# Performance work log

Hardware: AMD Instinct MI355X
Metric: run time of the kernel (lower is better)

Reference implementation:

```python
import jax, jax.numpy as jnp
import numpy as np

PARENTS = np.array([-1, 0, 1, 1, 1])
NECK_CHAIN = np.array([1, 0])  # neck joint (1) up to root (0)
B, V, F, J, S, E = 512, 5023, 9976, 5, 100, 50
L_STAT, L_DYN, L_FULL, N_BUCKET = 51, 17, 68, 79


def rodrigues(rvec):
    """Axis-angle [N,3] -> rotation matrices [N,3,3]."""
    angle = jnp.linalg.norm(rvec + 1e-8, axis=-1, keepdims=True)  # [N,1]
    axis = rvec / angle
    s = jnp.sin(angle)[..., None]
    c = jnp.cos(angle)[..., None]
    rx, ry, rz = axis[:, 0], axis[:, 1], axis[:, 2]
    z = jnp.zeros_like(rx)
    K = jnp.stack([z, -rz, ry, rz, z, -rx, -ry, rx, z], axis=-1).reshape(-1, 3, 3)
    I = jnp.eye(3, dtype=rvec.dtype)
    return I + s * K + (1.0 - c) * (K @ K)


def verts2lmk(vertices, faces, lmk_faces_idx, lmk_bary):
    lmk_faces = faces[lmk_faces_idx]                               # [B,L,3]
    lmk_verts = jax.vmap(lambda v, f: v[f])(vertices, lmk_faces)   # [B,L,3verts,3xyz]
    return jnp.einsum('blfc,blf->blc', lmk_verts, lmk_bary)


def setup_inputs() -> dict:
    key = jax.random.key(0)
    ks = jax.random.split(key, 16)
    shape_params = jax.random.normal(ks[0], (B, S), jnp.float32)
    expression_params = jax.random.normal(ks[1], (B, E), jnp.float32)
    pose_params = 0.2 * jax.random.normal(ks[2], (B, 6), jnp.float32)
    eye_pose_params = 0.1 * jax.random.normal(ks[3], (B, 6), jnp.float32)
    v_template = jax.random.normal(ks[4], (V, 3), jnp.float32) * 0.1
    shapedirs = jax.random.normal(ks[5], (V, 3, S + E), jnp.float32) * 0.01
    posedirs = jax.random.normal(ks[6], ((J - 1) * 9, V * 3), jnp.float32) * 0.01
    jr = jax.random.uniform(ks[7], (J, V), jnp.float32)
    J_regressor = jr / jnp.sum(jr, axis=1, keepdims=True)
    lbs_weights = jax.nn.softmax(jax.random.normal(ks[8], (V, J), jnp.float32), axis=-1)
    faces = jax.random.randint(ks[9], (F, 3), 0, V)
    lmk_faces_idx = jax.random.randint(ks[10], (L_STAT,), 0, F)
    lb = jax.random.uniform(ks[11], (L_STAT, 3), jnp.float32) + 1e-3
    lmk_bary_coords = lb / jnp.sum(lb, axis=-1, keepdims=True)
    dynamic_lmk_faces_idx = jax.random.randint(ks[12], (N_BUCKET, L_DYN), 0, F)
    db = jax.random.uniform(ks[13], (N_BUCKET, L_DYN, 3), jnp.float32) + 1e-3
    dynamic_lmk_bary_coords = db / jnp.sum(db, axis=-1, keepdims=True)
    full_lmk_faces_idx = jax.random.randint(ks[14], (L_FULL,), 0, F)
    fb = jax.random.uniform(ks[15], (L_FULL, 3), jnp.float32) + 1e-3
    full_lmk_bary_coords = fb / jnp.sum(fb, axis=-1, keepdims=True)
    return {
        'shape_params': shape_params, 'expression_params': expression_params,
        'pose_params': pose_params, 'eye_pose_params': eye_pose_params,
        'v_template': v_template, 'shapedirs': shapedirs, 'posedirs': posedirs,
        'J_regressor': J_regressor, 'lbs_weights': lbs_weights, 'faces': faces,
        'lmk_faces_idx': lmk_faces_idx, 'lmk_bary_coords': lmk_bary_coords,
        'dynamic_lmk_faces_idx': dynamic_lmk_faces_idx,
        'dynamic_lmk_bary_coords': dynamic_lmk_bary_coords,
        'full_lmk_faces_idx': full_lmk_faces_idx,
        'full_lmk_bary_coords': full_lmk_bary_coords,
    }


def reference(shape_params, expression_params, pose_params, eye_pose_params,
              v_template, shapedirs, posedirs, J_regressor, lbs_weights, faces,
              lmk_faces_idx, lmk_bary_coords, dynamic_lmk_faces_idx,
              dynamic_lmk_bary_coords, full_lmk_faces_idx, full_lmk_bary_coords):
    b = shape_params.shape[0]
    nv = v_template.shape[0]
    dt = shape_params.dtype
    betas = jnp.concatenate([shape_params, expression_params], axis=1)          # [B,150]
    neck = jnp.zeros((b, 3), dtype=dt)
    full_pose = jnp.concatenate(
        [pose_params[:, :3], neck, pose_params[:, 3:], eye_pose_params], axis=1)  # [B,15]
    # shape + expression blendshapes
    v_shaped = v_template[None] + jnp.einsum('bl,vcl->bvc', betas, shapedirs)   # [B,V,3]
    joints = jnp.einsum('jv,bvc->bjc', J_regressor, v_shaped)                   # [B,5,3]
    rot_mats = rodrigues(full_pose.reshape(-1, 3)).reshape(b, J, 3, 3)          # [B,5,3,3]
    I3 = jnp.eye(3, dtype=dt)
    pose_feature = (rot_mats[:, 1:] - I3).reshape(b, -1)                        # [B,36]
    v_posed = v_shaped + (pose_feature @ posedirs).reshape(b, nv, 3)
    # kinematic chain -> global joint transforms
    rel_J = joints.at[:, 1:].add(-joints[:, PARENTS[1:]])
    tm = jnp.zeros((b, J, 4, 4), dtype=dt)
    tm = tm.at[:, :, :3, :3].set(rot_mats).at[:, :, :3, 3].set(rel_J).at[:, :, 3, 3].set(1.0)
    chain = [tm[:, 0]]
    for i in range(1, J):
        chain.append(chain[PARENTS[i]] @ tm[:, i])
    A = jnp.stack(chain, axis=1)                                                # [B,5,4,4]
    Rj = jnp.einsum('bjmn,bjn->bjm', A[:, :, :3, :3], joints)
    A_rel = A.at[:, :, :3, 3].add(-Rj)
    # per-vertex skinning
    T = jnp.einsum('vj,bjmn->bvmn', lbs_weights, A_rel)                         # [B,V,4,4]
    vertices = jnp.einsum('bvmn,bvn->bvm', T[:, :, :3, :3], v_posed) + T[:, :, :3, 3]
    # dynamic contour landmark selection from neck kin-chain relative rotation
    aa = full_pose.reshape(b, J, 3)[:, NECK_CHAIN]                              # [B,2,3]
    rc = rodrigues(aa.reshape(-1, 3)).reshape(b, len(NECK_CHAIN), 3, 3)
    rel_rot = jnp.broadcast_to(I3, (b, 3, 3))
    for idx in range(len(NECK_CHAIN)):
        rel_rot = rc[:, idx] @ rel_rot
    sy = jnp.sqrt(rel_rot[:, 0, 0] ** 2 + rel_rot[:, 1, 0] ** 2)
    y_deg = jnp.arctan2(-rel_rot[:, 2, 0], sy) * (180.0 / np.pi)
    y_rot = jnp.round(jnp.minimum(y_deg, 39.0)).astype(jnp.int32)
    neg_mask = y_rot < 0
    big_neg = y_rot < -39
    neg_vals = jnp.where(big_neg, 78, 39 - y_rot)
    y_rot = jnp.where(neg_mask, neg_vals, y_rot)                                # [B] in [0,79)
    dyn_faces = dynamic_lmk_faces_idx[y_rot]                                    # [B,17]
    dyn_bary = dynamic_lmk_bary_coords[y_rot]                                   # [B,17,3]
    lf = jnp.concatenate([dyn_faces, jnp.broadcast_to(lmk_faces_idx[None], (b, lmk_faces_idx.shape[0]))], axis=1)
    lb = jnp.concatenate([dyn_bary, jnp.broadcast_to(lmk_bary_coords[None], (b,) + lmk_bary_coords.shape)], axis=1)
    landmarks2d = verts2lmk(vertices, faces, lf, lb)
    ff = jnp.broadcast_to(full_lmk_faces_idx[None], (b, full_lmk_faces_idx.shape[0]))
    fb = jnp.broadcast_to(full_lmk_bary_coords[None], (b,) + full_lmk_bary_coords.shape)
    landmarks3d = verts2lmk(vertices, faces, ff, fb)
    return (vertices, landmarks2d, landmarks3d)
```

## Files before the change

### kernel.cpp

```cpp
#include <hip/hip_runtime.h>
#include <cstddef>
#include <cstdint>

#define cB   512
#define cV   5023
#define cS   100
#define cE   50
#define cJ   5
#define cLD  17
#define cLF  68

#define cV3    15069
#define cNPAD  15072

#define OUT_V  ((size_t)cB * cV * 3)
#define OUT_L  ((size_t)cB * cLF * 3)

#define WS_BTN    ((size_t)0)
#define WS_ATM    (WS_BTN + (size_t)cNPAD * 96)
#define WS_JS2    (WS_ATM + 49152)
#define WS_AREL   (WS_JS2 + 2432)
#define WS_YROT   (WS_AREL + 30720)
#define WS_JSPART (WS_YROT + 512)

typedef __attribute__((ext_vector_type(8))) short short8;
typedef __attribute__((ext_vector_type(4))) float f32x4;

__device__ __forceinline__ unsigned short f2bf(float x) {
  unsigned int u = __float_as_uint(x);
  u = (u + 0x7fffu + ((u >> 16) & 1u)) >> 16;
  return (unsigned short)u;
}

__device__ __forceinline__ void rodrigues9(float rx, float ry, float rz, float* R) {
  float a0 = rx + 1e-8f, a1 = ry + 1e-8f, a2 = rz + 1e-8f;
  float angle = sqrtf(a0 * a0 + a1 * a1 + a2 * a2);
  float inv = 1.0f / angle;
  float x = rx * inv, y = ry * inv, z = rz * inv;
  float s = sinf(angle), c = cosf(angle);
  float t = 1.0f - c;
  float xy = x * y, xz = x * z, yz = y * z;
  R[0] = 1.0f - t * (y * y + z * z);
  R[1] = -s * z + t * xy;
  R[2] =  s * y + t * xz;
  R[3] =  s * z + t * xy;
  R[4] = 1.0f - t * (x * x + z * z);
  R[5] = -s * x + t * yz;
  R[6] = -s * y + t * xz;
  R[7] =  s * x + t * yz;
  R[8] = 1.0f - t * (x * x + y * y);
}

__global__ __launch_bounds__(512) void k_aux(
    const float* __restrict__ sd, const float* __restrict__ pd,
    const float* __restrict__ jreg, const float* __restrict__ vt,
    unsigned int* __restrict__ btn_u, float* __restrict__ JSpart) {
  __shared__ __align__(16) unsigned char sm[44032];
  float* sdt = (float*)sm;
  unsigned short* pdt = (unsigned short*)(sm + 38912);
  const int t = threadIdx.x;
  const int bid = blockIdx.x;
  if (bid < 314) {
    if (t >= 453) return;
    int c = t / 151, l = t - c * 151;
    int v0 = bid * 16;
    float acc[5] = {0.f, 0.f, 0.f, 0.f, 0.f};
#pragma unroll 8
    for (int vi = 0; vi < 16; ++vi) {
      int v = v0 + vi;
      bool ok = (v < cV);
      int vc = ok ? v : 0;
      float x;
      if (l < 150) x = ok ? sd[(size_t)(v * 3 + c) * 150 + l] : 0.f;
      else         x = ok ? vt[v * 3 + c] : 0.f;
#pragma unroll
      for (int j = 0; j < 5; ++j)
        acc[j] = fmaf(jreg[j * cV + vc], x, acc[j]);
    }
#pragma unroll
    for (int j = 0; j < 5; ++j)
      JSpart[(size_t)bid * 2272 + (j * 3 + c) * 151 + l] = acc[j];
  } else {
    const int n0 = (bid - 314) * 64;
    for (int idx = t; idx < 9600; idx += 512) {
      size_t g = (size_t)n0 * 150 + idx;
      float v = (g < (size_t)cV3 * 150) ? sd[g] : 0.f;
      int row = idx / 150, col = idx - row * 150;
      sdt[row * 152 + col] = v;
    }
    for (int e = t; e < 2304; e += 512) {
      int kk = e >> 6, ln = e & 63;
      int n = n0 + ln;
      pdt[ln * 38 + kk] = f2bf((n < cV3) ? pd[(size_t)kk * cV3 + n] : 0.f);
    }
    __syncthreads();
    for (int e = t; e < 6144; e += 512) {
      int row = e / 96, d = e - row * 96;
      int n = n0 + row;
      if (n < cNPAD) {
        unsigned int wv;
        if (d < 75) {
          wv = (unsigned int)f2bf(sdt[row * 152 + 2 * d]) |
               ((unsigned int)f2bf(sdt[row * 152 + 2 * d + 1]) << 16);
        } else if (d < 93) {
          int p = (d - 75) * 2;
          wv = (unsigned int)pdt[row * 38 + p] |
               ((unsigned int)pdt[row * 38 + p + 1] << 16);
        } else {
          wv = 0u;
        }
        btn_u[(size_t)n * 96 + d] = wv;
      }
    }
  }
}

__global__ __launch_bounds__(256) void k_jsred(const float* __restrict__ JSpart,
                                               float* __restrict__ JS2) {
  __shared__ float red[256];
  const int t = threadIdx.x;
  const int e = blockIdx.x * 32 + (t & 31);
  const int pg = t >> 5;
  float s = 0.f;
  if (e < 2265) {
#pragma unroll 8
    for (int p = pg; p < 314; p += 8)
      s += JSpart[(size_t)p * 2272 + e];
  }
  red[t] = s;
  __syncthreads();
  if (t < 128) red[t] += red[t + 128];
  __syncthreads();
  if (t < 64) red[t] += red[t + 64];
  __syncthreads();
  if (t < 32) {
    float v = red[t] + red[t + 32];
    if (e < 2265) {
      int jc = e / 151, l = e - jc * 151;
      JS2[l * 16 + jc] = v;
    }
  }
}

__global__ __launch_bounds__(256) void k_batch(
    const float* __restrict__ shp, const float* __restrict__ expr,
    const float* __restrict__ pose, const float* __restrict__ eyep,
    const float* __restrict__ JS2g, float* __restrict__ Arel,
    int* __restrict__ yrot, unsigned int* __restrict__ atm_u) {
  __shared__ float js2[151 * 16];
  __shared__ float sb[32 * 153];
  __shared__ float pfs[32 * 36];
  const int t = threadIdx.x;
  const int b0 = blockIdx.x * 32;
  for (int i = t; i < 151 * 16; i += 256) js2[i] = JS2g[i];
  for (int e = t; e < 3200; e += 256) {
    int bl = e / 100, l = e - bl * 100;
    sb[bl * 153 + l] = shp[(size_t)(b0 + bl) * 100 + l];
  }
  for (int e = t; e < 1600; e += 256) {
    int bl = e / 50, l = e - bl * 50;
    sb[bl * 153 + 100 + l] = expr[(size_t)(b0 + bl) * 50 + l];
  }
  __syncthreads();

  if (t < 32) {
    int b = b0 + t;
    float jnt[5][3];
    {
      const f32x4* J4 = (const f32x4*)(js2 + 150 * 16);
      f32x4 A = J4[0], Bq = J4[1], Cq = J4[2], Dq = J4[3];
      jnt[0][0] = A.x;  jnt[0][1] = A.y;  jnt[0][2] = A.z;
      jnt[1][0] = A.w;  jnt[1][1] = Bq.x; jnt[1][2] = Bq.y;
      jnt[2][0] = Bq.z; jnt[2][1] = Bq.w; jnt[2][2] = Cq.x;
      jnt[3][0] = Cq.y; jnt[3][1] = Cq.z; jnt[3][2] = Cq.w;
      jnt[4][0] = Dq.x; jnt[4][1] = Dq.y; jnt[4][2] = Dq.z;
    }
    for (int l = 0; l < 150; ++l) {
      const f32x4* J4 = (const f32x4*)(js2 + l * 16);
      f32x4 A = J4[0], Bq = J4[1], Cq = J4[2], Dq = J4[3];
      float beta = sb[t * 153 + l];
      jnt[0][0] = fmaf(beta, A.x,  jnt[0][0]);
      jnt[0][1] = fmaf(beta, A.y,  jnt[0][1]);
      jnt[0][2] = fmaf(beta, A.z,  jnt[0][2]);
      jnt[1][0] = fmaf(beta, A.w,  jnt[1][0]);
      jnt[1][1] = fmaf(beta, Bq.x, jnt[1][1]);
      jnt[1][2] = fmaf(beta, Bq.y, jnt[1][2]);
      jnt[2][0] = fmaf(beta, Bq.z, jnt[2][0]);
      jnt[2][1] = fmaf(beta, Bq.w, jnt[2][1]);
      jnt[2][2] = fmaf(beta, Cq.x, jnt[2][2]);
      jnt[3][0] = fmaf(beta, Cq.y, jnt[3][0]);
      jnt[3][1] = fmaf(beta, Cq.z, jnt[3][1]);
      jnt[3][2] = fmaf(beta, Cq.w, jnt[3][2]);
      jnt[4][0] = fmaf(beta, Dq.x, jnt[4][0]);
      jnt[4][1] = fmaf(beta, Dq.y, jnt[4][1]);
      jnt[4][2] = fmaf(beta, Dq.z, jnt[4][2]);
    }
    float fp[5][3];
    fp[0][0] = pose[b * 6 + 0]; fp[0][1] = pose[b * 6 + 1]; fp[0][2] = pose[b * 6 + 2];
    fp[1][0] = 0.f; fp[1][1] = 0.f; fp[1][2] = 0.f;
    fp[2][0] = pose[b * 6 + 3]; fp[2][1] = pose[b * 6 + 4]; fp[2][2] = pose[b * 6 + 5];
    fp[3][0] = eyep[b * 6 + 0]; fp[3][1] = eyep[b * 6 + 1]; fp[3][2] = eyep[b * 6 + 2];
    fp[4][0] = eyep[b * 6 + 3]; fp[4][1] = eyep[b * 6 + 4]; fp[4][2] = eyep[b * 6 + 5];
    float R[5][9];
#pragma unroll
    for (int j = 0; j < 5; ++j) rodrigues9(fp[j][0], fp[j][1], fp[j][2], R[j]);
#pragma unroll
    for (int j = 1; j < 5; ++j)
#pragma unroll
      for (int r = 0; r < 9; ++r) {
        float id = (r == 0 || r == 4 || r == 8) ? 1.f : 0.f;
        pfs[t * 36 + (j - 1) * 9 + r] = R[j][r] - id;
      }
    float rel[5][3];
#pragma unroll
    for (int c = 0; c < 3; ++c) {
      rel[0][c] = jnt[0][c];
      rel[1][c] = jnt[1][c] - jnt[0][c];
      rel[2][c] = jnt[2][c] - jnt[1][c];
      rel[3][c] = jnt[3][c] - jnt[1][c];
      rel[4][c] = jnt[4][c] - jnt[1][c];
    }
    float GR[5][9], Gt[5][3];
#pragma unroll
    for (int r = 0; r < 9; ++r) GR[0][r] = R[0][r];
#pragma unroll
    for (int c = 0; c < 3; ++c) Gt[0][c] = rel[0][c];
    const int par[5] = {0, 0, 1, 1, 1};
#pragma unroll
    for (int j = 1; j < 5; ++j) {
      int p = par[j];
#pragma unroll
      for (int r = 0; r < 3; ++r) {
#pragma unroll
        for (int cc = 0; cc < 3; ++cc)
          GR[j][r * 3 + cc] = GR[p][r * 3 + 0] * R[j][0 + cc] +
                              GR[p][r * 3 + 1] * R[j][3 + cc] +
                              GR[p][r * 3 + 2] * R[j][6 + cc];
        Gt[j][r] = Gt[p][r] + GR[p][r * 3 + 0] * rel[j][0] +
                              GR[p][r * 3 + 1] * rel[j][1] +
                              GR[p][r * 3 + 2] * rel[j][2];
      }
    }
#pragma unroll
    for (int j = 0; j < 5; ++j)
#pragma unroll
      for (int r = 0; r < 3; ++r) {
        float tj = Gt[j][r] - (GR[j][r * 3 + 0] * jnt[j][0] +
                               GR[j][r * 3 + 1] * jnt[j][1] +
                               GR[j][r * 3 + 2] * jnt[j][2]);
        Arel[b * 60 + j * 12 + r * 4 + 0] = GR[j][r * 3 + 0];
        Arel[b * 60 + j * 12 + r * 4 + 1] = GR[j][r * 3 + 1];
        Arel[b * 60 + j * 12 + r * 4 + 2] = GR[j][r * 3 + 2];
        Arel[b * 60 + j * 12 + r * 4 + 3] = tj;
      }
    float Ra[9], Rb[9];
    rodrigues9(fp[1][0], fp[1][1], fp[1][2], Ra);
    rodrigues9(fp[0][0], fp[0][1], fp[0][2], Rb);
    float r00 = Rb[0] * Ra[0] + Rb[1] * Ra[3] + Rb[2] * Ra[6];
    float r10 = Rb[3] * Ra[0] + Rb[4] * Ra[3] + Rb[5] * Ra[6];
    float r20 = Rb[6] * Ra[0] + Rb[7] * Ra[3] + Rb[8] * Ra[6];
    float sy = sqrtf(r00 * r00 + r10 * r10);
    float ydeg = atan2f(-r20, sy) * 57.29577951308232f;
    int y = (int)rintf(fminf(ydeg, 39.0f));
    if (y < 0) y = (y < -39) ? 78 : (39 - y);
    yrot[b] = y;
  }
  __syncthreads();

#pragma unroll
  for (int it = 0; it < 12; ++it) {
    int e = t + it * 256;
    int bl = e / 96, d = e - bl * 96;
    unsigned int wv;
    if (d < 75) {
      wv = (unsigned int)f2bf(sb[bl * 153 + 2 * d]) |
           ((unsigned int)f2bf(sb[bl * 153 + 2 * d + 1]) << 16);
    } else if (d < 93) {
      wv = (unsigned int)f2bf(pfs[bl * 36 + (d - 75) * 2]) |
           ((unsigned int)f2bf(pfs[bl * 36 + (d - 75) * 2 + 1]) << 16);
    } else {
      wv = 0u;
    }
    atm_u[(size_t)(b0 + bl) * 96 + d] = wv;
  }
}

__global__ __launch_bounds__(256) void k_main(
    const unsigned short* __restrict__ BTn, const unsigned short* __restrict__ ATm,
    const float* __restrict__ Arel, const float* __restrict__ vtempl,
    const float* __restrict__ lbw, float* __restrict__ out) {
  __shared__ __align__(16) unsigned char smem[39424];
  unsigned short* Bs = (unsigned short*)smem;
  float* Pf   = (float*)smem;
  float* lbwT = (float*)(smem + 38400);
  float* vtT  = (float*)(smem + 39040);

  const int bid = blockIdx.x;
  const int ph = bid >> 6, mb = (bid >> 3) & 7, r8 = bid & 7;
  const int p = ph * 8 + r8;

  const int t = threadIdx.x;
  const int w = t >> 6, L = t & 63;
  const int wm = w >> 1, wn = w & 1;
  const int lr = L & 15, lq = L >> 4;
  const int b_loc = t >> 2, part = t & 3;

  const float* qb = Arel + ((size_t)mb * 64 + b_loc) * 60;
  f32x4 ar[15];
#pragma unroll
  for (int r = 0; r < 15; ++r) ar[r] = *(const f32x4*)(qb + 4 * r);
  const unsigned short* abase = ATm + ((size_t)mb * 64 + wm * 32 + lr) * 192 + lq * 8;

#pragma unroll 1
  for (int i = 0; i < 2; ++i) {
    const int nb = 2 * p + i;
    if (nb >= 157) continue;
    if (i) __syncthreads();

    const unsigned short* bsrc = BTn + (size_t)nb * 96 * 192;
    uint4 bst[9];
#pragma unroll
    for (int it = 0; it < 9; ++it)
      bst[it] = *(const uint4*)(bsrc + ((size_t)(t + it * 256)) * 8);
#pragma unroll
    for (int it = 0; it < 9; ++it) {
      int e = t + it * 256;
      int row = e / 24, col = e - row * 24;
      *(uint4*)(smem + row * 400 + col * 16) = bst[it];
    }
    if (t < 160) {
      int vl = t / 5, j = t - vl * 5;
      int v = nb * 32 + vl;
      lbwT[t] = (v < cV) ? lbw[v * 5 + j] : 0.f;
    }
    if (t < 96) {
      int vl = t / 3, c = t - vl * 3;
      int v = nb * 32 + vl;
      vtT[t] = (v < cV) ? vtempl[v * 3 + c] : 0.f;
    }
    __syncthreads();

    f32x4 acc[2][3];
#pragma unroll
    for (int mt = 0; mt < 2; ++mt)
#pragma unroll
      for (int nt = 0; nt < 3; ++nt) acc[mt][nt] = (f32x4){0.f, 0.f, 0.f, 0.f};

    short8 af0 = *(const short8*)(abase);
    short8 af1 = *(const short8*)(abase + 16 * 192);
#pragma unroll
    for (int ks = 0; ks < 6; ++ks) {
      short8 nf0, nf1;
      if (ks < 5) {
        nf0 = *(const short8*)(abase + (ks + 1) * 32);
        nf1 = *(const short8*)(abase + 16 * 192 + (ks + 1) * 32);
      }
      const int ko = ks * 32 + lq * 8;
      short8 bf[3];
#pragma unroll
      for (int nt = 0; nt < 3; ++nt)
        bf[nt] = *(const short8*)(Bs + (wn * 48 + nt * 16 + lr) * 200 + ko);
#pragma unroll
      for (int nt = 0; nt < 3; ++nt) {
        acc[0][nt] = __builtin_amdgcn_mfma_f32_16x16x32_bf16(af0, bf[nt], acc[0][nt], 0, 0, 0);
        acc[1][nt] = __builtin_amdgcn_mfma_f32_16x16x32_bf16(af1, bf[nt], acc[1][nt], 0, 0, 0);
      }
      af0 = nf0; af1 = nf1;
    }
    __syncthreads();

#pragma unroll
    for (int mt = 0; mt < 2; ++mt)
#pragma unroll
      for (int nt = 0; nt < 3; ++nt) {
        int n_loc = wn * 48 + nt * 16 + lr;
        int m = wm * 32 + mt * 16 + lq * 4;
        *(f32x4*)(Pf + n_loc * 66 + m) = acc[mt][nt];
      }
    __syncthreads();

#pragma unroll
    for (int ii = 0; ii < 8; ++ii) {
      const int vl = part * 8 + ii;
      float px = Pf[(vl * 3 + 0) * 66 + b_loc] + vtT[vl * 3 + 0];
      float py = Pf[(vl * 3 + 1) * 66 + b_loc] + vtT[vl * 3 + 1];
      float pz = Pf[(vl * 3 + 2) * 66 + b_loc] + vtT[vl * 3 + 2];
      float o0 = 0.f, o1 = 0.f, o2 = 0.f;
#pragma unroll
      for (int j = 0; j < 5; ++j) {
        f32x4 q0 = ar[3 * j + 0], q1 = ar[3 * j + 1], q2 = ar[3 * j + 2];
        float s0 = q0.x * px + q0.y * py + q0.z * pz + q0.w;
        float s1 = q1.x * px + q1.y * py + q1.z * pz + q1.w;
        float s2 = q2.x * px + q2.y * py + q2.z * pz + q2.w;
        float wj = lbwT[vl * 5 + j];
        o0 = fmaf(wj, s0, o0);
        o1 = fmaf(wj, s1, o1);
        o2 = fmaf(wj, s2, o2);
      }
      const int v = nb * 32 + vl;
      if (v < cV) {
        size_t off = ((size_t)(mb * 64 + b_loc) * cV + v) * 3;
        out[off + 0] = o0;
        out[off + 1] = o1;
        out[off + 2] = o2;
      }
    }
  }
}

__global__ __launch_bounds__(512) void k_lmk(
    const float* __restrict__ verts, const int* __restrict__ faces,
    const int* __restrict__ lmkf, const float* __restrict__ lmkb,
    const int* __restrict__ dynf, const float* __restrict__ dynb,
    const int* __restrict__ fullf, const float* __restrict__ fullb,
    const int* __restrict__ yrot, float* __restrict__ out) {
  int id = blockIdx.x * 512 + threadIdx.x;
  if (id >= cB * cLF * 2) return;
  int sel = id & 1;
  int r = id >> 1;
  int b = r / cLF, l = r - b * cLF;
  const float* vb = verts + (size_t)b * cV * 3;
  int f; float w0, w1, w2; size_t o;
  if (sel == 0) {
    if (l < cLD) {
      int yb = yrot[b];
      f = dynf[yb * cLD + l];
      const float* bp = dynb + ((size_t)yb * cLD + l) * 3;
      w0 = bp[0]; w1 = bp[1]; w2 = bp[2];
    } else {
      f = lmkf[l - cLD];
      const float* bp = lmkb + (size_t)(l - cLD) * 3;
      w0 = bp[0]; w1 = bp[1]; w2 = bp[2];
    }
    o = OUT_V + ((size_t)b * cLF + l) * 3;
  } else {
    f = fullf[l];
    const float* bp = fullb + (size_t)l * 3;
    w0 = bp[0]; w1 = bp[1]; w2 = bp[2];
    o = OUT_V + OUT_L + ((size_t)b * cLF + l) * 3;
  }
  int i0 = faces[f * 3 + 0] * 3, i1 = faces[f * 3 + 1] * 3, i2 = faces[f * 3 + 2] * 3;
  out[o + 0] = w0 * vb[i0 + 0] + w1 * vb[i1 + 0] + w2 * vb[i2 + 0];
  out[o + 1] = w0 * vb[i0 + 1] + w1 * vb[i1 + 1] + w2 * vb[i2 + 1];
  out[o + 2] = w0 * vb[i0 + 2] + w1 * vb[i1 + 2] + w2 * vb[i2 + 2];
}

extern "C" void kernel_launch(void* const* d_in, const int* in_sizes, int n_in,
                              void* d_out, int out_size, void* d_ws, size_t ws_size,
                              hipStream_t stream) {
  (void)in_sizes; (void)n_in; (void)out_size; (void)ws_size;
  const float* shp  = (const float*)d_in[0];
  const float* expr = (const float*)d_in[1];
  const float* pose = (const float*)d_in[2];
  const float* eyep = (const float*)d_in[3];
  const float* vt   = (const float*)d_in[4];
  const float* sd   = (const float*)d_in[5];
  const float* pd   = (const float*)d_in[6];
  const float* jreg = (const float*)d_in[7];
  const float* lbw  = (const float*)d_in[8];
  const int*   fcs  = (const int*)d_in[9];
  const int*   lmkf = (const int*)d_in[10];
  const float* lmkb = (const float*)d_in[11];
  const int*   dynf = (const int*)d_in[12];
  const float* dynb = (const float*)d_in[13];
  const int*   fullf= (const int*)d_in[14];
  const float* fullb= (const float*)d_in[15];
  float* out = (float*)d_out;
  float* ws  = (float*)d_ws;

  unsigned int*   btn  = (unsigned int*)(ws + WS_BTN);
  unsigned short* ATm  = (unsigned short*)(ws + WS_ATM);
  float* JS2    = ws + WS_JS2;
  float* Arel   = ws + WS_AREL;
  int*   yrot   = (int*)(ws + WS_YROT);
  float* JSpart = ws + WS_JSPART;

  k_aux<<<550, 512, 0, stream>>>(sd, pd, jreg, vt, btn, JSpart);
  k_jsred<<<71, 256, 0, stream>>>(JSpart, JS2);
  k_batch<<<16, 256, 0, stream>>>(shp, expr, pose, eyep, JS2, Arel, yrot,
                                  (unsigned int*)ATm);
  k_main<<<640, 256, 0, stream>>>((unsigned short*)btn, ATm, Arel, vt, lbw, out);
  k_lmk<<<136, 512, 0, stream>>>(out, fcs, lmkf, lmkb, dynf, dynb, fullf, fullb, yrot, out);
}
```

Measured before the change: 181.2 us.

## Stage skinned output in LDS for coalesced stores and one tile per block

```diff
diff --git a/kernel.cpp b/kernel.cpp
--- a/kernel.cpp
+++ b/kernel.cpp
@@ -285,106 +285,110 @@
   }
 }
 
-__global__ __launch_bounds__(256) void k_main(
+__global__ __launch_bounds__(256, 4) void k_main(
     const unsigned short* __restrict__ BTn, const unsigned short* __restrict__ ATm,
     const float* __restrict__ Arel, const float* __restrict__ vtempl,
     const float* __restrict__ lbw, float* __restrict__ out) {
   __shared__ __align__(16) unsigned char smem[39424];
   unsigned short* Bs = (unsigned short*)smem;
   float* Pf   = (float*)smem;
+  float* Os   = (float*)(smem + 25344);
   float* lbwT = (float*)(smem + 38400);
   float* vtT  = (float*)(smem + 39040);
 
   const int bid = blockIdx.x;
-  const int ph = bid >> 6, mb = (bid >> 3) & 7, r8 = bid & 7;
-  const int p = ph * 8 + r8;
+  const int xcd = bid & 7, slot = bid >> 3;
+  const int nb = xcd * 20 + (slot >> 3);
+  const int mb = slot & 7;
+  if (nb >= 157) return;
 
   const int t = threadIdx.x;
   const int w = t >> 6, L = t & 63;
   const int wm = w >> 1, wn = w & 1;
   const int lr = L & 15, lq = L >> 4;
-  const int b_loc = t >> 2, part = t & 3;
-
-  const float* qb = Arel + ((size_t)mb * 64 + b_loc) * 60;
-  f32x4 ar[15];
-#pragma unroll
-  for (int r = 0; r < 15; ++r) ar[r] = *(const f32x4*)(qb + 4 * r);
+
+  const unsigned short* bsrc = BTn + (size_t)nb * 96 * 192;
+  uint4 bst[9];
+#pragma unroll
+  for (int it = 0; it < 9; ++it)
+    bst[it] = *(const uint4*)(bsrc + ((size_t)(t + it * 256)) * 8);
+#pragma unroll
+  for (int it = 0; it < 9; ++it) {
+    int e = t + it * 256;
+    int row = e / 24, col = e - row * 24;
+    *(uint4*)(smem + row * 400 + col * 16) = bst[it];
+  }
+  if (t < 160) {
+    int vl = t / 5, j = t - vl * 5;
+    int v = nb * 32 + vl;
+    lbwT[t] = (v < cV) ? lbw[v * 5 + j] : 0.f;
+  }
+  if (t < 96) {
+    int vl = t / 3, c = t - vl * 3;
+    int v = nb * 32 + vl;
+    vtT[t] = (v < cV) ? vtempl[v * 3 + c] : 0.f;
+  }
+  __syncthreads();
+
+  f32x4 acc[2][3];
+#pragma unroll
+  for (int mt = 0; mt < 2; ++mt)
+#pragma unroll
+    for (int nt = 0; nt < 3; ++nt) acc[mt][nt] = (f32x4){0.f, 0.f, 0.f, 0.f};
+
   const unsigned short* abase = ATm + ((size_t)mb * 64 + wm * 32 + lr) * 192 + lq * 8;
-
+  short8 af0 = *(const short8*)(abase);
+  short8 af1 = *(const short8*)(abase + 16 * 192);
+#pragma unroll
+  for (int ks = 0; ks < 6; ++ks) {
+    short8 nf0, nf1;
+    if (ks < 5) {
+      nf0 = *(const short8*)(abase + (ks + 1) * 32);
+      nf1 = *(const short8*)(abase + 16 * 192 + (ks + 1) * 32);
+    }
+    const int ko = ks * 32 + lq * 8;
+    short8 bf[3];
+#pragma unroll
+    for (int nt = 0; nt < 3; ++nt)
+      bf[nt] = *(const short8*)(Bs + (wn * 48 + nt * 16 + lr) * 200 + ko);
+#pragma unroll
+    for (int nt = 0; nt < 3; ++nt) {
+      acc[0][nt] = __builtin_amdgcn_mfma_f32_16x16x32_bf16(af0, bf[nt], acc[0][nt], 0, 0, 0);
+      acc[1][nt] = __builtin_amdgcn_mfma_f32_16x16x32_bf16(af1, bf[nt], acc[1][nt], 0, 0, 0);
+    }
+    af0 = nf0; af1 = nf1;
+  }
+  __syncthreads();
+
+#pragma unroll
+  for (int mt = 0; mt < 2; ++mt)
+#pragma unroll
+    for (int nt = 0; nt < 3; ++nt) {
+      int n_loc = wn * 48 + nt * 16 + lr;
+      int m = wm * 32 + mt * 16 + lq * 4;
+      *(f32x4*)(Pf + n_loc * 66 + m) = acc[mt][nt];
+    }
+  __syncthreads();
+
+  const int bq = t >> 3, vt8 = t & 7;
+  const size_t cv3 = (size_t)cV * 3;
 #pragma unroll 1
-  for (int i = 0; i < 2; ++i) {
-    const int nb = 2 * p + i;
-    if (nb >= 157) continue;
-    if (i) __syncthreads();
-
-    const unsigned short* bsrc = BTn + (size_t)nb * 96 * 192;
-    uint4 bst[9];
-#pragma unroll
-    for (int it = 0; it < 9; ++it)
-      bst[it] = *(const uint4*)(bsrc + ((size_t)(t + it * 256)) * 8);
-#pragma unroll
-    for (int it = 0; it < 9; ++it) {
-      int e = t + it * 256;
-      int row = e / 24, col = e - row * 24;
-      *(uint4*)(smem + row * 400 + col * 16) = bst[it];
-    }
-    if (t < 160) {
-      int vl = t / 5, j = t - vl * 5;
-      int v = nb * 32 + vl;
-      lbwT[t] = (v < cV) ? lbw[v * 5 + j] : 0.f;
-    }
-    if (t < 96) {
-      int vl = t / 3, c = t - vl * 3;
-      int v = nb * 32 + vl;
-      vtT[t] = (v < cV) ? vtempl[v * 3 + c] : 0.f;
-    }
-    __syncthreads();
-
-    f32x4 acc[2][3];
-#pragma unroll
-    for (int mt = 0; mt < 2; ++mt)
-#pragma unroll
-      for (int nt = 0; nt < 3; ++nt) acc[mt][nt] = (f32x4){0.f, 0.f, 0.f, 0.f};
-
-    short8 af0 = *(const short8*)(abase);
-    short8 af1 = *(const short8*)(abase + 16 * 192);
-#pragma unroll
-    for (int ks = 0; ks < 6; ++ks) {
-      short8 nf0, nf1;
-      if (ks < 5) {
-        nf0 = *(const short8*)(abase + (ks + 1) * 32);
-        nf1 = *(const short8*)(abase + 16 * 192 + (ks + 1) * 32);
-      }
-      const int ko = ks * 32 + lq * 8;
-      short8 bf[3];
-#pragma unroll
-      for (int nt = 0; nt < 3; ++nt)
-        bf[nt] = *(const short8*)(Bs + (wn * 48 + nt * 16 + lr) * 200 + ko);
-#pragma unroll
-      for (int nt = 0; nt < 3; ++nt) {
-        acc[0][nt] = __builtin_amdgcn_mfma_f32_16x16x32_bf16(af0, bf[nt], acc[0][nt], 0, 0, 0);
-        acc[1][nt] = __builtin_amdgcn_mfma_f32_16x16x32_bf16(af1, bf[nt], acc[1][nt], 0, 0, 0);
-      }
-      af0 = nf0; af1 = nf1;
-    }
-    __syncthreads();
-
-#pragma unroll
-    for (int mt = 0; mt < 2; ++mt)
-#pragma unroll
-      for (int nt = 0; nt < 3; ++nt) {
-        int n_loc = wn * 48 + nt * 16 + lr;
-        int m = wm * 32 + mt * 16 + lq * 4;
-        *(f32x4*)(Pf + n_loc * 66 + m) = acc[mt][nt];
-      }
-    __syncthreads();
-
-#pragma unroll
-    for (int ii = 0; ii < 8; ++ii) {
-      const int vl = part * 8 + ii;
-      float px = Pf[(vl * 3 + 0) * 66 + b_loc] + vtT[vl * 3 + 0];
-      float py = Pf[(vl * 3 + 1) * 66 + b_loc] + vtT[vl * 3 + 1];
-      float pz = Pf[(vl * 3 + 2) * 66 + b_loc] + vtT[vl * 3 + 2];
+  for (int h = 0; h < 2; ++h) {
+    if (h) __syncthreads();
+    const int bcol = h * 32 + bq;
+    const int b = mb * 64 + bcol;
+    const float* qb = Arel + (size_t)b * 60;
+    f32x4 ar[15];
+#pragma unroll
+    for (int r = 0; r < 15; ++r) ar[r] = *(const f32x4*)(qb + 4 * r);
+
+    float o12[12];
+#pragma unroll
+    for (int i = 0; i < 4; ++i) {
+      const int vl = vt8 * 4 + i;
+      float px = Pf[(vl * 3 + 0) * 66 + bcol] + vtT[vl * 3 + 0];
+      float py = Pf[(vl * 3 + 1) * 66 + bcol] + vtT[vl * 3 + 1];
+      float pz = Pf[(vl * 3 + 2) * 66 + bcol] + vtT[vl * 3 + 2];
       float o0 = 0.f, o1 = 0.f, o2 = 0.f;
 #pragma unroll
       for (int j = 0; j < 5; ++j) {
@@ -397,13 +401,23 @@
         o1 = fmaf(wj, s1, o1);
         o2 = fmaf(wj, s2, o2);
       }
-      const int v = nb * 32 + vl;
-      if (v < cV) {
-        size_t off = ((size_t)(mb * 64 + b_loc) * cV + v) * 3;
-        out[off + 0] = o0;
-        out[off + 1] = o1;
-        out[off + 2] = o2;
-      }
+      o12[i * 3 + 0] = o0; o12[i * 3 + 1] = o1; o12[i * 3 + 2] = o2;
+    }
+    {
+      float* op = Os + bq * 96 + vt8 * 12;
+      *(f32x4*)(op + 0) = (f32x4){o12[0], o12[1], o12[2],  o12[3]};
+      *(f32x4*)(op + 4) = (f32x4){o12[4], o12[5], o12[6],  o12[7]};
+      *(f32x4*)(op + 8) = (f32x4){o12[8], o12[9], o12[10], o12[11]};
+    }
+    __syncthreads();
+
+    const size_t ob = ((size_t)(mb * 64 + h * 32) * cV + (size_t)nb * 32) * 3;
+#pragma unroll
+    for (int s = 0; s < 12; ++s) {
+      int idx = s * 256 + t;
+      int bb = idx / 96, f = idx - bb * 96;
+      if (nb < 156 || f < 93)
+        out[ob + (size_t)bb * cv3 + f] = Os[idx];
     }
   }
 }
@@ -479,6 +493,6 @@
   k_jsred<<<71, 256, 0, stream>>>(JSpart, JS2);
   k_batch<<<16, 256, 0, stream>>>(shp, expr, pose, eyep, JS2, Arel, yrot,
                                   (unsigned int*)ATm);
-  k_main<<<640, 256, 0, stream>>>((unsigned short*)btn, ATm, Arel, vt, lbw, out);
+  k_main<<<1280, 256, 0, stream>>>((unsigned short*)btn, ATm, Arel, vt, lbw, out);
   k_lmk<<<136, 512, 0, stream>>>(out, fcs, lmkf, lmkb, dynf, dynb, fullf, fullb, yrot, out);
 }
```

Result: slower. 230.1 us (+26.9%).

## Load B fragments directly from global and give each block a single N tile

Applied to the files above, without the earlier changes.

```diff
diff --git a/kernel.cpp b/kernel.cpp
--- a/kernel.cpp
+++ b/kernel.cpp
@@ -289,121 +289,106 @@
     const unsigned short* __restrict__ BTn, const unsigned short* __restrict__ ATm,
     const float* __restrict__ Arel, const float* __restrict__ vtempl,
     const float* __restrict__ lbw, float* __restrict__ out) {
-  __shared__ __align__(16) unsigned char smem[39424];
-  unsigned short* Bs = (unsigned short*)smem;
-  float* Pf   = (float*)smem;
-  float* lbwT = (float*)(smem + 38400);
-  float* vtT  = (float*)(smem + 39040);
+  __shared__ float Pf[96 * 66];
+  __shared__ float lbwT[160];
+  __shared__ float vtT[96];
 
   const int bid = blockIdx.x;
-  const int ph = bid >> 6, mb = (bid >> 3) & 7, r8 = bid & 7;
-  const int p = ph * 8 + r8;
+  const int nb = bid >> 3, mb = bid & 7;
 
   const int t = threadIdx.x;
   const int w = t >> 6, L = t & 63;
   const int wm = w >> 1, wn = w & 1;
   const int lr = L & 15, lq = L >> 4;
+
+  if (t < 160) {
+    int vl = t / 5, j = t - vl * 5;
+    int v = nb * 32 + vl;
+    lbwT[t] = (v < cV) ? lbw[v * 5 + j] : 0.f;
+  }
+  if (t >= 160 && t < 256) {
+    int e = t - 160;
+    int vl = e / 3, c = e - vl * 3;
+    int v = nb * 32 + vl;
+    vtT[e] = (v < cV) ? vtempl[v * 3 + c] : 0.f;
+  }
+
+  const unsigned short* abase = ATm + ((size_t)mb * 64 + wm * 32 + lr) * 192 + lq * 8;
+  const unsigned short* bbase = BTn + ((size_t)nb * 96 + wn * 48 + lr) * 192 + lq * 8;
+
+  f32x4 acc[2][3];
+#pragma unroll
+  for (int mt = 0; mt < 2; ++mt)
+#pragma unroll
+    for (int nt = 0; nt < 3; ++nt) acc[mt][nt] = (f32x4){0.f, 0.f, 0.f, 0.f};
+
+  short8 af0 = *(const short8*)(abase);
+  short8 af1 = *(const short8*)(abase + 16 * 192);
+  short8 bf0 = *(const short8*)(bbase);
+  short8 bf1 = *(const short8*)(bbase + 16 * 192);
+  short8 bf2 = *(const short8*)(bbase + 32 * 192);
+#pragma unroll
+  for (int ks = 0; ks < 6; ++ks) {
+    short8 naf0, naf1, nbf0, nbf1, nbf2;
+    if (ks < 5) {
+      const int ko = (ks + 1) * 32;
+      naf0 = *(const short8*)(abase + ko);
+      naf1 = *(const short8*)(abase + 16 * 192 + ko);
+      nbf0 = *(const short8*)(bbase + ko);
+      nbf1 = *(const short8*)(bbase + 16 * 192 + ko);
+      nbf2 = *(const short8*)(bbase + 32 * 192 + ko);
+    }
+    acc[0][0] = __builtin_amdgcn_mfma_f32_16x16x32_bf16(af0, bf0, acc[0][0], 0, 0, 0);
+    acc[1][0] = __builtin_amdgcn_mfma_f32_16x16x32_bf16(af1, bf0, acc[1][0], 0, 0, 0);
+    acc[0][1] = __builtin_amdgcn_mfma_f32_16x16x32_bf16(af0, bf1, acc[0][1], 0, 0, 0);
+    acc[1][1] = __builtin_amdgcn_mfma_f32_16x16x32_bf16(af1, bf1, acc[1][1], 0, 0, 0);
+    acc[0][2] = __builtin_amdgcn_mfma_f32_16x16x32_bf16(af0, bf2, acc[0][2], 0, 0, 0);
+    acc[1][2] = __builtin_amdgcn_mfma_f32_16x16x32_bf16(af1, bf2, acc[1][2], 0, 0, 0);
+    af0 = naf0; af1 = naf1; bf0 = nbf0; bf1 = nbf1; bf2 = nbf2;
+  }
+
+#pragma unroll
+  for (int mt = 0; mt < 2; ++mt)
+#pragma unroll
+    for (int nt = 0; nt < 3; ++nt) {
+      int n_loc = wn * 48 + nt * 16 + lr;
+      int m = wm * 32 + mt * 16 + lq * 4;
+      *(f32x4*)(Pf + n_loc * 66 + m) = acc[mt][nt];
+    }
+
   const int b_loc = t >> 2, part = t & 3;
-
   const float* qb = Arel + ((size_t)mb * 64 + b_loc) * 60;
   f32x4 ar[15];
 #pragma unroll
   for (int r = 0; r < 15; ++r) ar[r] = *(const f32x4*)(qb + 4 * r);
-  const unsigned short* abase = ATm + ((size_t)mb * 64 + wm * 32 + lr) * 192 + lq * 8;
-
-#pragma unroll 1
-  for (int i = 0; i < 2; ++i) {
-    const int nb = 2 * p + i;
-    if (nb >= 157) continue;
-    if (i) __syncthreads();
-
-    const unsigned short* bsrc = BTn + (size_t)nb * 96 * 192;
-    uint4 bst[9];
-#pragma unroll
-    for (int it = 0; it < 9; ++it)
-      bst[it] = *(const uint4*)(bsrc + ((size_t)(t + it * 256)) * 8);
-#pragma unroll
-    for (int it = 0; it < 9; ++it) {
-      int e = t + it * 256;
-      int row = e / 24, col = e - row * 24;
-      *(uint4*)(smem + row * 400 + col * 16) = bst[it];
-    }
-    if (t < 160) {
-      int vl = t / 5, j = t - vl * 5;
-      int v = nb * 32 + vl;
-      lbwT[t] = (v < cV) ? lbw[v * 5 + j] : 0.f;
-    }
-    if (t < 96) {
-      int vl = t / 3, c = t - vl * 3;
-      int v = nb * 32 + vl;
-      vtT[t] = (v < cV) ? vtempl[v * 3 + c] : 0.f;
-    }
-    __syncthreads();
-
-    f32x4 acc[2][3];
-#pragma unroll
-    for (int mt = 0; mt < 2; ++mt)
-#pragma unroll
-      for (int nt = 0; nt < 3; ++nt) acc[mt][nt] = (f32x4){0.f, 0.f, 0.f, 0.f};
-
-    short8 af0 = *(const short8*)(abase);
-    short8 af1 = *(const short8*)(abase + 16 * 192);
-#pragma unroll
-    for (int ks = 0; ks < 6; ++ks) {
-      short8 nf0, nf1;
-      if (ks < 5) {
-        nf0 = *(const short8*)(abase + (ks + 1) * 32);
-        nf1 = *(const short8*)(abase + 16 * 192 + (ks + 1) * 32);
-      }
-      const int ko = ks * 32 + lq * 8;
-      short8 bf[3];
-#pragma unroll
-      for (int nt = 0; nt < 3; ++nt)
-        bf[nt] = *(const short8*)(Bs + (wn * 48 + nt * 16 + lr) * 200 + ko);
-#pragma unroll
-      for (int nt = 0; nt < 3; ++nt) {
-        acc[0][nt] = __builtin_amdgcn_mfma_f32_16x16x32_bf16(af0, bf[nt], acc[0][nt], 0, 0, 0);
-        acc[1][nt] = __builtin_amdgcn_mfma_f32_16x16x32_bf16(af1, bf[nt], acc[1][nt], 0, 0, 0);
-      }
-      af0 = nf0; af1 = nf1;
-    }
-    __syncthreads();
-
-#pragma unroll
-    for (int mt = 0; mt < 2; ++mt)
-#pragma unroll
-      for (int nt = 0; nt < 3; ++nt) {
-        int n_loc = wn * 48 + nt * 16 + lr;
-        int m = wm * 32 + mt * 16 + lq * 4;
-        *(f32x4*)(Pf + n_loc * 66 + m) = acc[mt][nt];
-      }
-    __syncthreads();
-
-#pragma unroll
-    for (int ii = 0; ii < 8; ++ii) {
-      const int vl = part * 8 + ii;
-      float px = Pf[(vl * 3 + 0) * 66 + b_loc] + vtT[vl * 3 + 0];
-      float py = Pf[(vl * 3 + 1) * 66 + b_loc] + vtT[vl * 3 + 1];
-      float pz = Pf[(vl * 3 + 2) * 66 + b_loc] + vtT[vl * 3 + 2];
-      float o0 = 0.f, o1 = 0.f, o2 = 0.f;
-#pragma unroll
-      for (int j = 0; j < 5; ++j) {
-        f32x4 q0 = ar[3 * j + 0], q1 = ar[3 * j + 1], q2 = ar[3 * j + 2];
-        float s0 = q0.x * px + q0.y * py + q0.z * pz + q0.w;
-        float s1 = q1.x * px + q1.y * py + q1.z * pz + q1.w;
-        float s2 = q2.x * px + q2.y * py + q2.z * pz + q2.w;
-        float wj = lbwT[vl * 5 + j];
-        o0 = fmaf(wj, s0, o0);
-        o1 = fmaf(wj, s1, o1);
-        o2 = fmaf(wj, s2, o2);
-      }
-      const int v = nb * 32 + vl;
-      if (v < cV) {
-        size_t off = ((size_t)(mb * 64 + b_loc) * cV + v) * 3;
-        out[off + 0] = o0;
-        out[off + 1] = o1;
-        out[off + 2] = o2;
-      }
+
+  __syncthreads();
+
+  const size_t cv3 = (size_t)cV * 3;
+#pragma unroll
+  for (int ii = 0; ii < 8; ++ii) {
+    const int vl = part * 8 + ii;
+    float px = Pf[(vl * 3 + 0) * 66 + b_loc] + vtT[vl * 3 + 0];
+    float py = Pf[(vl * 3 + 1) * 66 + b_loc] + vtT[vl * 3 + 1];
+    float pz = Pf[(vl * 3 + 2) * 66 + b_loc] + vtT[vl * 3 + 2];
+    float o0 = 0.f, o1 = 0.f, o2 = 0.f;
+#pragma unroll
+    for (int j = 0; j < 5; ++j) {
+      f32x4 q0 = ar[3 * j + 0], q1 = ar[3 * j + 1], q2 = ar[3 * j + 2];
+      float s0 = q0.x * px + q0.y * py + q0.z * pz + q0.w;
+      float s1 = q1.x * px + q1.y * py + q1.z * pz + q1.w;
+      float s2 = q2.x * px + q2.y * py + q2.z * pz + q2.w;
+      float wj = lbwT[vl * 5 + j];
+      o0 = fmaf(wj, s0, o0);
+      o1 = fmaf(wj, s1, o1);
+      o2 = fmaf(wj, s2, o2);
+    }
+    const int v = nb * 32 + vl;
+    if (v < cV) {
+      size_t off = ((size_t)(mb * 64 + b_loc) * cV + v) * 3;
+      out[off + 0] = o0;
+      out[off + 1] = o1;
+      out[off + 2] = o2;
     }
   }
 }
@@ -479,6 +464,6 @@
   k_jsred<<<71, 256, 0, stream>>>(JSpart, JS2);
   k_batch<<<16, 256, 0, stream>>>(shp, expr, pose, eyep, JS2, Arel, yrot,
                                   (unsigned int*)ATm);
-  k_main<<<640, 256, 0, stream>>>((unsigned short*)btn, ATm, Arel, vt, lbw, out);
+  k_main<<<1256, 256, 0, stream>>>((unsigned short*)btn, ATm, Arel, vt, lbw, out);
   k_lmk<<<136, 512, 0, stream>>>(out, fcs, lmkf, lmkb, dynf, dynb, fullf, fullb, yrot, out);
 }
```

Measured after the change: 177.0 us. -2.4%, faster.
